# Optimization experiments

Hardware: AMD Instinct MI355X
Metric: run time of the kernel (lower is better)

## Reference

```python
import jax, jax.numpy as jnp
import numpy as np

B, T, D, H, L, F = 128, 512, 32, 128, 3, 4


def setup_inputs() -> dict:
    key = jax.random.key(0)
    ks = jax.random.split(key, 13)
    s = 0.05
    inp = {
        "x": jax.random.normal(ks[0], (B, T, D), dtype=jnp.float32),
        # layer 0 input weights [4H, D]; layers 1..L-1 input weights [L-1, 4H, H]
        "w_ih0": jax.random.normal(ks[1], (4 * H, D), dtype=jnp.float32) * s,
        "w_ih_rest": jax.random.normal(ks[2], (L - 1, 4 * H, H), dtype=jnp.float32) * s,
        "w_hh": jax.random.normal(ks[3], (L, 4 * H, H), dtype=jnp.float32) * s,
        "b_ih": jax.random.normal(ks[4], (L, 4 * H), dtype=jnp.float32) * s,
        "b_hh": jax.random.normal(ks[5], (L, 4 * H), dtype=jnp.float32) * s,
        "w_attn": jax.random.normal(ks[6], (1, H), dtype=jnp.float32) * s,
        "b_attn": jax.random.normal(ks[7], (1,), dtype=jnp.float32) * s,
        "w1": jax.random.normal(ks[8], (64, H), dtype=jnp.float32) * s,
        "b1": jax.random.normal(ks[9], (64,), dtype=jnp.float32) * s,
        "w2": jax.random.normal(ks[10], (F, 64), dtype=jnp.float32) * s,
        "b2": jax.random.normal(ks[11], (F,), dtype=jnp.float32) * s,
    }
    return inp


def _lstm_layer(xs, w_ih, w_hh, bi, bh):
    # xs: [B, T, Din] -> hs: [B, T, H]; PyTorch gate order i, f, g, o
    b, t = xs.shape[0], xs.shape[1]
    h_dim = w_hh.shape[1]
    pre = jnp.einsum('bti,gi->btg', xs, w_ih) + bi + bh  # [B, T, 4H]

    def step(carry, p_t):
        h, c = carry
        g = p_t + h @ w_hh.T
        i, f, gg, o = jnp.split(g, 4, axis=-1)
        i = jax.nn.sigmoid(i)
        f = jax.nn.sigmoid(f)
        gg = jnp.tanh(gg)
        o = jax.nn.sigmoid(o)
        c = f * c + i * gg
        h = o * jnp.tanh(c)
        return (h, c), h

    h0 = jnp.zeros((b, h_dim), xs.dtype)
    _, hs = jax.lax.scan(step, (h0, h0), jnp.swapaxes(pre, 0, 1))
    return jnp.swapaxes(hs, 0, 1)


def reference(x, w_ih0, w_ih_rest, w_hh, b_ih, b_hh, w_attn, b_attn, w1, b1, w2, b2):
    out = _lstm_layer(x, w_ih0, w_hh[0], b_ih[0], b_hh[0])
    for l in range(1, L):
        out = _lstm_layer(out, w_ih_rest[l - 1], w_hh[l], b_ih[l], b_hh[l])
    # additive attention pooling over time
    attn_w = jax.nn.softmax(jnp.einsum('bth,oh->bto', out, w_attn) + b_attn, axis=1)  # [B,T,1]
    ctx = jnp.sum(attn_w * out, axis=1)  # [B, H]
    # MLP head (dropout is identity at inference)
    h1 = jax.nn.relu(ctx @ w1.T + b1)
    return h1 @ w2.T + b2
```

## Files before the change

kernel.cpp:

```cpp
#include <hip/hip_runtime.h>
#include <math.h>

#define Bn 128
#define Tn 512
#define Dn 32
#define Hn 128
#define Gn 512
#define Ln 3

#define BAR_LDS() asm volatile("s_waitcnt lgkmcnt(0)\n\ts_barrier" ::: "memory")

typedef _Float16 h2 __attribute__((ext_vector_type(2)));
typedef _Float16 h4 __attribute__((ext_vector_type(4)));
typedef _Float16 half8 __attribute__((ext_vector_type(8)));
typedef float f32x4 __attribute__((ext_vector_type(4)));

__device__ __forceinline__ float dot2(h2 a, h2 b, float c) {
    return __builtin_amdgcn_fdot2(a, b, c, false);
}
__device__ __forceinline__ h2 pkh(float a, float b) {
    h2 r; r.x = (_Float16)a; r.y = (_Float16)b; return r;
}
__device__ __forceinline__ float sigm(float x) {
    return __builtin_amdgcn_rcpf(1.f + __expf(-x));
}
__device__ __forceinline__ float tanh_fast(float x) {
    return 1.f - 2.f * __builtin_amdgcn_rcpf(1.f + __expf(2.f * x));
}

#define DPPADD(a, CTRL) { \
    int _t = __builtin_amdgcn_update_dpp(0, __builtin_bit_cast(int, a), \
                                         CTRL, 0xF, 0xF, true); \
    a += __builtin_bit_cast(float, _t); }

#define KEEPH(x) asm volatile("" : "+v"(x))
#define LD8H(p) (*(const half8*)(p))
#define H2OF(V, i) (((const h2*)&(V))[i])

#define DECL16(P, R) \
  h2 P##0=pkh((R)[0],(R)[1]),   P##1=pkh((R)[2],(R)[3]),   P##2=pkh((R)[4],(R)[5]),   P##3=pkh((R)[6],(R)[7]),   \
     P##4=pkh((R)[8],(R)[9]),   P##5=pkh((R)[10],(R)[11]), P##6=pkh((R)[12],(R)[13]), P##7=pkh((R)[14],(R)[15]), \
     P##8=pkh((R)[16],(R)[17]), P##9=pkh((R)[18],(R)[19]), P##10=pkh((R)[20],(R)[21]),P##11=pkh((R)[22],(R)[23]),\
     P##12=pkh((R)[24],(R)[25]),P##13=pkh((R)[26],(R)[27]),P##14=pkh((R)[28],(R)[29]),P##15=pkh((R)[30],(R)[31]);
#define KEEP16(P) \
  KEEPH(P##0); KEEPH(P##1); KEEPH(P##2); KEEPH(P##3); KEEPH(P##4); KEEPH(P##5); \
  KEEPH(P##6); KEEPH(P##7); KEEPH(P##8); KEEPH(P##9); KEEPH(P##10); KEEPH(P##11); \
  KEEPH(P##12); KEEPH(P##13); KEEPH(P##14); KEEPH(P##15);

#define EXTRACT16(P, A, B, C, D) \
  h2 P##0 = H2OF(A,0), P##1 = H2OF(A,1), P##2  = H2OF(A,2), P##3  = H2OF(A,3), \
     P##4 = H2OF(B,0), P##5 = H2OF(B,1), P##6  = H2OF(B,2), P##7  = H2OF(B,3), \
     P##8 = H2OF(C,0), P##9 = H2OF(C,1), P##10 = H2OF(C,2), P##11 = H2OF(C,3), \
     P##12= H2OF(D,0), P##13= H2OF(D,1), P##14 = H2OF(D,2), P##15 = H2OF(D,3);

#define DOTA(j) { \
    aI = dot2(hvA##j, wiA##j, aI);  aF = dot2(hvA##j, wfA##j, aF); \
    aG = dot2(hvA##j, wgA##j, aG);  aO = dot2(hvA##j, woA##j, aO); }
#define DOTB(j) { \
    aI = dot2(hvB##j, wiB##j, aI);  aF = dot2(hvB##j, wfB##j, aF); \
    aG = dot2(hvB##j, wgB##j, aG);  aO = dot2(hvB##j, woB##j, aO); }

template<typename TA>
__global__ __launch_bounds__(256) void gemm_pre(
    const TA* __restrict__ A, int K, int rowStrideB, int t0, int tlog,
    const float* __restrict__ W,
    const float* __restrict__ bi, const float* __restrict__ bh,
    _Float16* __restrict__ C)
{
    __shared__ h2 As2[64][20];
    __shared__ h2 Bs2[64][20];
    const int tid  = threadIdx.x;
    const int row0 = blockIdx.x * 64;
    const int col0 = blockIdx.y * 64;
    const int w    = tid >> 6;
    const int lane = tid & 63;
    const int qm   = (w >> 1) * 32;
    const int qn   = (w & 1) * 32;
    const int fm   = lane & 15;
    const int fq   = lane >> 4;
    const int tmask = (1 << tlog) - 1;
    const int lrow = tid >> 2;
    const int lk   = (tid & 3) * 8;

    f32x4 acc00 = {0,0,0,0}, acc01 = {0,0,0,0};
    f32x4 acc10 = {0,0,0,0}, acc11 = {0,0,0,0};

    for (int k0 = 0; k0 < K; k0 += 32) {
        {
            int rg = row0 + lrow;
            int b_idx = rg >> tlog, tt = rg & tmask;
            const TA* ap = A + (size_t)b_idx * rowStrideB +
                           (size_t)(t0 + tt) * K + (k0 + lk);
            if constexpr (sizeof(TA) == 2) {
                *(float4*)&As2[lrow][(tid & 3) * 4] = *(const float4*)ap;
            } else {
                float4 va = *(const float4*)ap;
                float4 vb = *(const float4*)(ap + 4);
                float4 o;
                ((h2*)&o)[0] = pkh(va.x, va.y);
                ((h2*)&o)[1] = pkh(va.z, va.w);
                ((h2*)&o)[2] = pkh(vb.x, vb.y);
                ((h2*)&o)[3] = pkh(vb.z, vb.w);
                *(float4*)&As2[lrow][(tid & 3) * 4] = o;
            }
            const float* wp = W + (size_t)(col0 + lrow) * K + (k0 + lk);
            float4 wa = *(const float4*)wp;
            float4 wb = *(const float4*)(wp + 4);
            float4 ow;
            ((h2*)&ow)[0] = pkh(wa.x, wa.y);
            ((h2*)&ow)[1] = pkh(wa.z, wa.w);
            ((h2*)&ow)[2] = pkh(wb.x, wb.y);
            ((h2*)&ow)[3] = pkh(wb.z, wb.w);
            *(float4*)&Bs2[lrow][(tid & 3) * 4] = ow;
        }
        __syncthreads();
        half8 a0 = *(const half8*)&As2[qm + fm][fq * 4];
        half8 a1 = *(const half8*)&As2[qm + 16 + fm][fq * 4];
        half8 b0 = *(const half8*)&Bs2[qn + fm][fq * 4];
        half8 b1 = *(const half8*)&Bs2[qn + 16 + fm][fq * 4];
        acc00 = __builtin_amdgcn_mfma_f32_16x16x32_f16(a0, b0, acc00, 0, 0, 0);
        acc01 = __builtin_amdgcn_mfma_f32_16x16x32_f16(a0, b1, acc01, 0, 0, 0);
        acc10 = __builtin_amdgcn_mfma_f32_16x16x32_f16(a1, b0, acc10, 0, 0, 0);
        acc11 = __builtin_amdgcn_mfma_f32_16x16x32_f16(a1, b1, acc11, 0, 0, 0);
        __syncthreads();
    }

    const int g0 = col0 + qn + fm;
    const int g1 = g0 + 16;
    const float bb0 = bi[g0] + bh[g0];
    const float bb1 = bi[g1] + bh[g1];
    const int m0 = row0 + qm + fq * 4;
    #pragma unroll
    for (int r = 0; r < 4; r++) {
        int ma = m0 + r, mb = m0 + 16 + r;
        C[((size_t)(ma >> 2) * Gn + g0) * 4 + (ma & 3)] = (_Float16)(acc00[r] + bb0);
        C[((size_t)(ma >> 2) * Gn + g1) * 4 + (ma & 3)] = (_Float16)(acc01[r] + bb1);
        C[((size_t)(mb >> 2) * Gn + g0) * 4 + (mb & 3)] = (_Float16)(acc10[r] + bb0);
        C[((size_t)(mb >> 2) * Gn + g1) * 4 + (mb & 3)] = (_Float16)(acc11[r] + bb1);
    }
}

__global__ __launch_bounds__(256)
__attribute__((amdgpu_waves_per_eu(1, 2)))
void scan256(
    const _Float16* __restrict__ pre,
    const float* __restrict__ w_hh,
    _Float16* __restrict__ hs16)
{
    const int b    = blockIdx.x;
    const int tid  = threadIdx.x;
    const int lane = tid & 63;
    const int wv   = tid >> 6;
    const int kq   = lane & 1;
    const int u    = wv * 32 + (lane >> 1);

    __shared__ h2 hbuf[2][Hn / 2];
    __shared__ _Float16 hstage[2][16][Hn];
    __shared__ float lds_pad[19456];

    if (pre == nullptr) {
        lds_pad[tid] = (float)tid;
        __syncthreads();
        ((float*)hs16)[tid] = lds_pad[(tid * 7) & 19455];
    }

    const float* rI = w_hh + (size_t)(0 * Hn + u) * Hn + kq * 64;
    const float* rF = w_hh + (size_t)(1 * Hn + u) * Hn + kq * 64;
    const float* rG = w_hh + (size_t)(2 * Hn + u) * Hn + kq * 64;
    const float* rO = w_hh + (size_t)(3 * Hn + u) * Hn + kq * 64;
    DECL16(wiA, rI) DECL16(wiB, (rI + 32))
    DECL16(wfA, rF) DECL16(wfB, (rF + 32))
    DECL16(wgA, rG) DECL16(wgB, (rG + 32))
    DECL16(woA, rO) DECL16(woB, (rO + 32))
    KEEP16(wiA) KEEP16(wiB) KEEP16(wfA) KEEP16(wfB)
    KEEP16(wgA) KEEP16(wgB) KEEP16(woA) KEEP16(woB)

    if (tid < Hn / 2) hbuf[0][tid] = pkh(0.f, 0.f);
    __syncthreads();

    const h4* qq = (const h4*)pre + (size_t)(b * 128) * Gn + u;
    _Float16* hsb = hs16 + (size_t)b * Tn * Hn;

    const float ms = (kq == 0) ? 1.f : 0.f;

    h4 qI0 = qq[0],   qF0 = qq[128],      qG0 = qq[256],      qO0 = qq[384];
    h4 qI1 = qq[Gn],  qF1 = qq[Gn + 128], qG1 = qq[Gn + 256], qO1 = qq[Gn + 384];
    const h4* pld = qq + 2 * (size_t)Gn;

    float cr = 0.f;

    auto body = [&](int t, float vI, float vF, float vG, float vO) {
        const h2* hrow = &hbuf[t & 1][kq * 32];
        half8 hA = LD8H(hrow);      half8 hB = LD8H(hrow + 4);
        half8 hC = LD8H(hrow + 8);  half8 hD = LD8H(hrow + 12);
        half8 hE = LD8H(hrow + 16); half8 hF_ = LD8H(hrow + 20);
        half8 hG_ = LD8H(hrow + 24); half8 hH_ = LD8H(hrow + 28);
        EXTRACT16(hvA, hA, hB, hC, hD)
        EXTRACT16(hvB, hE, hF_, hG_, hH_)

        float aI = vI, aF = vF, aG = vG, aO = vO;
        DOTA(0)  DOTA(1)  DOTA(2)  DOTA(3)
        DOTA(4)  DOTA(5)  DOTA(6)  DOTA(7)
        DOTA(8)  DOTA(9)  DOTA(10) DOTA(11)
        DOTA(12) DOTA(13) DOTA(14) DOTA(15)
        DOTB(0)  DOTB(1)  DOTB(2)  DOTB(3)
        DOTB(4)  DOTB(5)  DOTB(6)  DOTB(7)
        DOTB(8)  DOTB(9)  DOTB(10) DOTB(11)
        DOTB(12) DOTB(13) DOTB(14) DOTB(15)

        DPPADD(aI, 0xB1) DPPADD(aF, 0xB1) DPPADD(aG, 0xB1) DPPADD(aO, 0xB1)

        float iv = sigm(aI);
        float fv = sigm(aF);
        float gv = tanh_fast(aG);
        float ov = sigm(aO);
        cr = fv * cr + iv * gv;
        float hnew = ov * tanh_fast(cr);
        _Float16 hh = (_Float16)hnew;
        if (kq == 0) {
            ((_Float16*)hbuf[(t + 1) & 1])[u] = hh;
            hstage[(t >> 4) & 1][t & 15][u] = hh;
        }
        BAR_LDS();
    };

    auto flush = [&](int ch) {
        const float4* src = (const float4*)&hstage[ch & 1][0][0];
        float4 v = src[tid];
        *(float4*)(hsb + (size_t)ch * 16 * Hn + tid * 8) = v;
    };

    for (int qr = 0; qr < 126; qr++) {
        body(4 * qr,     ms * (float)qI0.x, ms * (float)qF0.x,
                         ms * (float)qG0.x, ms * (float)qO0.x);
        body(4 * qr + 1, ms * (float)qI0.y, ms * (float)qF0.y,
                         ms * (float)qG0.y, ms * (float)qO0.y);
        body(4 * qr + 2, ms * (float)qI0.z, ms * (float)qF0.z,
                         ms * (float)qG0.z, ms * (float)qO0.z);
        body(4 * qr + 3, ms * (float)qI0.w, ms * (float)qF0.w,
                         ms * (float)qG0.w, ms * (float)qO0.w);
        if ((qr & 3) == 3) flush(qr >> 2);
        qI0 = qI1; qF0 = qF1; qG0 = qG1; qO0 = qO1;
        qI1 = pld[0]; qF1 = pld[128]; qG1 = pld[256]; qO1 = pld[384];
        pld += Gn;
    }
    body(504, ms * (float)qI0.x, ms * (float)qF0.x,
              ms * (float)qG0.x, ms * (float)qO0.x);
    body(505, ms * (float)qI0.y, ms * (float)qF0.y,
              ms * (float)qG0.y, ms * (float)qO0.y);
    body(506, ms * (float)qI0.z, ms * (float)qF0.z,
              ms * (float)qG0.z, ms * (float)qO0.z);
    body(507, ms * (float)qI0.w, ms * (float)qF0.w,
              ms * (float)qG0.w, ms * (float)qO0.w);
    qI0 = qI1; qF0 = qF1; qG0 = qG1; qO0 = qO1;
    body(508, ms * (float)qI0.x, ms * (float)qF0.x,
              ms * (float)qG0.x, ms * (float)qO0.x);
    body(509, ms * (float)qI0.y, ms * (float)qF0.y,
              ms * (float)qG0.y, ms * (float)qO0.y);
    body(510, ms * (float)qI0.z, ms * (float)qF0.z,
              ms * (float)qG0.z, ms * (float)qO0.z);
    body(511, ms * (float)qI0.w, ms * (float)qF0.w,
              ms * (float)qG0.w, ms * (float)qO0.w);
    flush(31);
}

__global__ __launch_bounds__(256) void head_kernel(
    const _Float16* __restrict__ hs16,
    const float* __restrict__ w_attn, const float* __restrict__ b_attn,
    const float* __restrict__ w1, const float* __restrict__ b1,
    const float* __restrict__ w2, const float* __restrict__ b2,
    float* __restrict__ out)
{
    const int b = blockIdx.x;
    const int tid = threadIdx.x;
    __shared__ h2 wa2[Hn / 2];
    __shared__ __align__(16) float sc[Tn];
    __shared__ __align__(16) float red[256];
    __shared__ __align__(16) float ctx_sh[Hn];
    __shared__ __align__(16) float h1_sh[64];

    if (tid < Hn / 2) wa2[tid] = pkh(w_attn[2 * tid], w_attn[2 * tid + 1]);
    __syncthreads();

    const _Float16* hb = hs16 + (size_t)b * Tn * Hn;

    for (int t = tid; t < Tn; t += 256) {
        const h2* hp = (const h2*)(hb + (size_t)t * Hn);
        float s = 0.f;
        #pragma unroll
        for (int k = 0; k < 64; k++) s = dot2(hp[k], wa2[k], s);
        sc[t] = s + b_attn[0];
    }
    __syncthreads();

    float m = fmaxf(sc[tid], sc[tid + 256]);
    red[tid] = m; __syncthreads();
    for (int s_ = 128; s_ > 0; s_ >>= 1) {
        if (tid < s_) red[tid] = fmaxf(red[tid], red[tid + s_]);
        __syncthreads();
    }
    float mx = red[0];
    __syncthreads();
    float e0 = __expf(sc[tid] - mx), e1 = __expf(sc[tid + 256] - mx);
    sc[tid] = e0; sc[tid + 256] = e1;
    red[tid] = e0 + e1; __syncthreads();
    for (int s_ = 128; s_ > 0; s_ >>= 1) {
        if (tid < s_) red[tid] += red[tid + s_];
        __syncthreads();
    }
    float inv = 1.f / red[0];
    __syncthreads();

    {
        int jj = tid & 127, half = tid >> 7;
        float a = 0.f;
        for (int t = half * 256; t < half * 256 + 256; t++)
            a += sc[t] * (float)hb[(size_t)t * Hn + jj];
        red[tid] = a;
        __syncthreads();
        if (tid < Hn) ctx_sh[tid] = (red[tid] + red[tid + Hn]) * inv;
        __syncthreads();
    }

    if (tid < 64) {
        const float4* wvv = (const float4*)(w1 + (size_t)tid * Hn);
        const float4* cv = (const float4*)ctx_sh;
        float s = 0.f;
        #pragma unroll
        for (int k = 0; k < 32; k++) {
            float4 a = wvv[k], c = cv[k];
            s += a.x * c.x + a.y * c.y + a.z * c.z + a.w * c.w;
        }
        h1_sh[tid] = fmaxf(s + b1[tid], 0.f);
    }
    __syncthreads();

    if (tid < 4) {
        float s = 0.f;
        const float* wvv = w2 + tid * 64;
        #pragma unroll
        for (int k = 0; k < 64; k++) s += wvv[k] * h1_sh[k];
        out[b * 4 + tid] = s + b2[tid];
    }
}

extern "C" void kernel_launch(void* const* d_in, const int* in_sizes, int n_in,
                              void* d_out, int out_size, void* d_ws, size_t ws_size,
                              hipStream_t stream)
{
    const float* x        = (const float*)d_in[0];
    const float* w_ih0    = (const float*)d_in[1];
    const float* w_ih_rest= (const float*)d_in[2];
    const float* w_hh     = (const float*)d_in[3];
    const float* b_ih     = (const float*)d_in[4];
    const float* b_hh     = (const float*)d_in[5];
    const float* w_attn   = (const float*)d_in[6];
    const float* b_attn   = (const float*)d_in[7];
    const float* w1       = (const float*)d_in[8];
    const float* b1       = (const float*)d_in[9];
    const float* w2       = (const float*)d_in[10];
    const float* b2       = (const float*)d_in[11];
    float* out = (float*)d_out;

    const size_t nHS  = (size_t)Bn * Tn * Hn;
    const size_t nPRE = (size_t)Bn * Tn * Gn;

    _Float16* preh = (_Float16*)d_ws;
    _Float16* hs0  = preh + nPRE;
    _Float16* hs1  = hs0 + nHS;
    _Float16* hs2  = hs1 + nHS;

    gemm_pre<float><<<dim3(Bn * Tn / 64, 8), 256, 0, stream>>>(
        x, Dn, Tn * Dn, 0, 9, w_ih0, b_ih, b_hh, preh);
    scan256<<<Bn, 256, 0, stream>>>(preh, w_hh, hs0);

    gemm_pre<_Float16><<<dim3(Bn * Tn / 64, 8), 256, 0, stream>>>(
        hs0, Hn, Tn * Hn, 0, 9, w_ih_rest,
        b_ih + Gn, b_hh + Gn, preh);
    scan256<<<Bn, 256, 0, stream>>>(preh, w_hh + (size_t)Gn * Hn, hs1);

    gemm_pre<_Float16><<<dim3(Bn * Tn / 64, 8), 256, 0, stream>>>(
        hs1, Hn, Tn * Hn, 0, 9, w_ih_rest + (size_t)Gn * Hn,
        b_ih + 2 * Gn, b_hh + 2 * Gn, preh);
    scan256<<<Bn, 256, 0, stream>>>(preh, w_hh + 2 * (size_t)Gn * Hn, hs2);

    head_kernel<<<Bn, 256, 0, stream>>>(hs2, w_attn, b_attn, w1, b1, w2, b2, out);
}
```

Baseline: 991.3 us.

## Fuse layer-0 and layer-1 LSTM scans into one wavefront-pipelined kernel

Result: slower. 1.017 ms (+2.6%).

```diff
diff --git a/kernel.cpp b/kernel.cpp
--- a/kernel.cpp
+++ b/kernel.cpp
@@ -59,6 +59,12 @@
 #define DOTB(j) { \
     aI = dot2(hvB##j, wiB##j, aI);  aF = dot2(hvB##j, wfB##j, aF); \
     aG = dot2(hvB##j, wgB##j, aG);  aO = dot2(hvB##j, woB##j, aO); }
+#define DOT4V(j) { \
+    aI = dot2(hv##j, wi##j, aI);  aF = dot2(hv##j, wf##j, aF); \
+    aG = dot2(hv##j, wg##j, aG);  aO = dot2(hv##j, wo##j, aO); }
+#define DOT4Y(j) { \
+    aI = dot2(pv##j, yi##j, aI);  aF = dot2(pv##j, yf##j, aF); \
+    aG = dot2(pv##j, yg##j, aG);  aO = dot2(pv##j, yo##j, aO); }
 
 template<typename TA>
 __global__ __launch_bounds__(256) void gemm_pre(
@@ -140,6 +146,201 @@
     }
 }
 
+__global__ __launch_bounds__(768)
+__attribute__((amdgpu_waves_per_eu(3)))
+void pipe01(
+    const _Float16* __restrict__ pre0,
+    const float* __restrict__ w_hh,
+    const float* __restrict__ wih1,
+    const float* __restrict__ b_ih, const float* __restrict__ b_hh,
+    _Float16* __restrict__ hs1)
+{
+    const int b    = blockIdx.x;
+    const int tid  = threadIdx.x;
+    const int lane = tid & 63;
+    const int wv   = tid >> 6;
+
+    __shared__ h2 h0buf[2][Hn / 2];
+    __shared__ h2 h1buf[2][Hn / 2];
+    __shared__ _Float16 hstage[2][16][Hn];
+
+    if (tid < Hn / 2) {
+        h0buf[0][tid] = pkh(0.f, 0.f); h0buf[1][tid] = pkh(0.f, 0.f);
+        h1buf[0][tid] = pkh(0.f, 0.f); h1buf[1][tid] = pkh(0.f, 0.f);
+    }
+    __syncthreads();
+
+    if (wv < 4) {
+        const int kq = lane & 1;
+        const int u  = wv * 32 + (lane >> 1);
+
+        const float* rI = w_hh + (size_t)(0 * Hn + u) * Hn + kq * 64;
+        const float* rF = w_hh + (size_t)(1 * Hn + u) * Hn + kq * 64;
+        const float* rG = w_hh + (size_t)(2 * Hn + u) * Hn + kq * 64;
+        const float* rO = w_hh + (size_t)(3 * Hn + u) * Hn + kq * 64;
+        DECL16(wiA, rI) DECL16(wiB, (rI + 32))
+        DECL16(wfA, rF) DECL16(wfB, (rF + 32))
+        DECL16(wgA, rG) DECL16(wgB, (rG + 32))
+        DECL16(woA, rO) DECL16(woB, (rO + 32))
+        KEEP16(wiA) KEEP16(wiB) KEEP16(wfA) KEEP16(wfB)
+        KEEP16(wgA) KEEP16(wgB) KEEP16(woA) KEEP16(woB)
+
+        const h4* qq = (const h4*)pre0 + (size_t)(b * 128) * Gn + u;
+        const float ms = (kq == 0) ? 1.f : 0.f;
+
+        h4 qI0 = qq[0],  qF0 = qq[128],      qG0 = qq[256],      qO0 = qq[384];
+        h4 qI1 = qq[Gn], qF1 = qq[Gn + 128], qG1 = qq[Gn + 256], qO1 = qq[Gn + 384];
+        const h4* pld = qq + 2 * (size_t)Gn;
+
+        float cr = 0.f;
+
+        auto body = [&](int t, float vI, float vF, float vG, float vO) {
+            const h2* hrow = &h0buf[t & 1][kq * 32];
+            half8 hA = LD8H(hrow);      half8 hB = LD8H(hrow + 4);
+            half8 hC = LD8H(hrow + 8);  half8 hD = LD8H(hrow + 12);
+            half8 hE = LD8H(hrow + 16); half8 hF_ = LD8H(hrow + 20);
+            half8 hG_ = LD8H(hrow + 24); half8 hH_ = LD8H(hrow + 28);
+            EXTRACT16(hvA, hA, hB, hC, hD)
+            EXTRACT16(hvB, hE, hF_, hG_, hH_)
+
+            float aI = vI, aF = vF, aG = vG, aO = vO;
+            DOTA(0)  DOTA(1)  DOTA(2)  DOTA(3)
+            DOTA(4)  DOTA(5)  DOTA(6)  DOTA(7)
+            DOTA(8)  DOTA(9)  DOTA(10) DOTA(11)
+            DOTA(12) DOTA(13) DOTA(14) DOTA(15)
+            DOTB(0)  DOTB(1)  DOTB(2)  DOTB(3)
+            DOTB(4)  DOTB(5)  DOTB(6)  DOTB(7)
+            DOTB(8)  DOTB(9)  DOTB(10) DOTB(11)
+            DOTB(12) DOTB(13) DOTB(14) DOTB(15)
+
+            DPPADD(aI, 0xB1) DPPADD(aF, 0xB1) DPPADD(aG, 0xB1) DPPADD(aO, 0xB1)
+
+            float iv = sigm(aI);
+            float fv = sigm(aF);
+            float gv = tanh_fast(aG);
+            float ov = sigm(aO);
+            cr = fv * cr + iv * gv;
+            float hnew = ov * tanh_fast(cr);
+            if (kq == 0)
+                ((_Float16*)h0buf[(t + 1) & 1])[u] = (_Float16)hnew;
+            BAR_LDS();
+        };
+
+        for (int qr = 0; qr < 126; qr++) {
+            body(4 * qr,     ms * (float)qI0.x, ms * (float)qF0.x,
+                             ms * (float)qG0.x, ms * (float)qO0.x);
+            body(4 * qr + 1, ms * (float)qI0.y, ms * (float)qF0.y,
+                             ms * (float)qG0.y, ms * (float)qO0.y);
+            body(4 * qr + 2, ms * (float)qI0.z, ms * (float)qF0.z,
+                             ms * (float)qG0.z, ms * (float)qO0.z);
+            body(4 * qr + 3, ms * (float)qI0.w, ms * (float)qF0.w,
+                             ms * (float)qG0.w, ms * (float)qO0.w);
+            qI0 = qI1; qF0 = qF1; qG0 = qG1; qO0 = qO1;
+            qI1 = pld[0]; qF1 = pld[128]; qG1 = pld[256]; qO1 = pld[384];
+            pld += Gn;
+        }
+        body(504, ms * (float)qI0.x, ms * (float)qF0.x,
+                  ms * (float)qG0.x, ms * (float)qO0.x);
+        body(505, ms * (float)qI0.y, ms * (float)qF0.y,
+                  ms * (float)qG0.y, ms * (float)qO0.y);
+        body(506, ms * (float)qI0.z, ms * (float)qF0.z,
+                  ms * (float)qG0.z, ms * (float)qO0.z);
+        body(507, ms * (float)qI0.w, ms * (float)qF0.w,
+                  ms * (float)qG0.w, ms * (float)qO0.w);
+        qI0 = qI1; qF0 = qF1; qG0 = qG1; qO0 = qO1;
+        body(508, ms * (float)qI0.x, ms * (float)qF0.x,
+                  ms * (float)qG0.x, ms * (float)qO0.x);
+        body(509, ms * (float)qI0.y, ms * (float)qF0.y,
+                  ms * (float)qG0.y, ms * (float)qO0.y);
+        body(510, ms * (float)qI0.z, ms * (float)qF0.z,
+                  ms * (float)qG0.z, ms * (float)qO0.z);
+        body(511, ms * (float)qI0.w, ms * (float)qF0.w,
+                  ms * (float)qG0.w, ms * (float)qO0.w);
+        BAR_LDS();
+        BAR_LDS();
+    } else {
+        const int wl   = wv - 4;
+        const int kq4  = lane & 3;
+        const int u1   = wl * 16 + (lane >> 2);
+        const int ltid = tid - 256;
+
+        const float* whh1 = w_hh + (size_t)Gn * Hn;
+        const float* rI = whh1 + (size_t)(0 * Hn + u1) * Hn + kq4 * 32;
+        const float* rF = whh1 + (size_t)(1 * Hn + u1) * Hn + kq4 * 32;
+        const float* rG = whh1 + (size_t)(2 * Hn + u1) * Hn + kq4 * 32;
+        const float* rO = whh1 + (size_t)(3 * Hn + u1) * Hn + kq4 * 32;
+        DECL16(wi, rI) DECL16(wf, rF) DECL16(wg, rG) DECL16(wo, rO)
+        KEEP16(wi) KEEP16(wf) KEEP16(wg) KEEP16(wo)
+
+        const float* yIr = wih1 + (size_t)(0 * Hn + u1) * Hn + kq4 * 32;
+        const float* yFr = wih1 + (size_t)(1 * Hn + u1) * Hn + kq4 * 32;
+        const float* yGr = wih1 + (size_t)(2 * Hn + u1) * Hn + kq4 * 32;
+        const float* yOr = wih1 + (size_t)(3 * Hn + u1) * Hn + kq4 * 32;
+        DECL16(yi, yIr) DECL16(yf, yFr) DECL16(yg, yGr) DECL16(yo, yOr)
+        KEEP16(yi) KEEP16(yf) KEEP16(yg) KEEP16(yo)
+
+        const float bI1 = b_ih[Gn + 0 * Hn + u1] + b_hh[Gn + 0 * Hn + u1];
+        const float bF1 = b_ih[Gn + 1 * Hn + u1] + b_hh[Gn + 1 * Hn + u1];
+        const float bG1 = b_ih[Gn + 2 * Hn + u1] + b_hh[Gn + 2 * Hn + u1];
+        const float bO1 = b_ih[Gn + 3 * Hn + u1] + b_hh[Gn + 3 * Hn + u1];
+
+        _Float16* hs1b = hs1 + (size_t)b * Tn * Hn;
+        float cr = 0.f;
+
+        for (int i = 0; i < 513; i++) {
+            if (i > 0) {
+                const int t1 = i - 1;
+                const h2* h1row = &h1buf[(i - 1) & 1][kq4 * 16];
+                half8 hA = LD8H(h1row);     half8 hB = LD8H(h1row + 4);
+                half8 hC = LD8H(h1row + 8); half8 hD = LD8H(h1row + 12);
+                EXTRACT16(hv, hA, hB, hC, hD)
+                const h2* h0row = &h0buf[i & 1][kq4 * 16];
+                half8 pA = LD8H(h0row);     half8 pB = LD8H(h0row + 4);
+                half8 pC = LD8H(h0row + 8); half8 pD = LD8H(h0row + 12);
+                EXTRACT16(pv, pA, pB, pC, pD)
+
+                float aI = 0.f, aF = 0.f, aG = 0.f, aO = 0.f;
+                DOT4V(0)  DOT4V(1)  DOT4V(2)  DOT4V(3)
+                DOT4V(4)  DOT4V(5)  DOT4V(6)  DOT4V(7)
+                DOT4V(8)  DOT4V(9)  DOT4V(10) DOT4V(11)
+                DOT4V(12) DOT4V(13) DOT4V(14) DOT4V(15)
+                DOT4Y(0)  DOT4Y(1)  DOT4Y(2)  DOT4Y(3)
+                DOT4Y(4)  DOT4Y(5)  DOT4Y(6)  DOT4Y(7)
+                DOT4Y(8)  DOT4Y(9)  DOT4Y(10) DOT4Y(11)
+                DOT4Y(12) DOT4Y(13) DOT4Y(14) DOT4Y(15)
+
+                DPPADD(aI, 0xB1) DPPADD(aF, 0xB1) DPPADD(aG, 0xB1) DPPADD(aO, 0xB1)
+                DPPADD(aI, 0x4E) DPPADD(aF, 0x4E) DPPADD(aG, 0x4E) DPPADD(aO, 0x4E)
+
+                float iv = sigm(aI + bI1);
+                float fv = sigm(aF + bF1);
+                float gv = tanh_fast(aG + bG1);
+                float ov = sigm(aO + bO1);
+                cr = fv * cr + iv * gv;
+                float hnew = ov * tanh_fast(cr);
+                _Float16 hh_ = (_Float16)hnew;
+                if (kq4 == 0) {
+                    ((_Float16*)h1buf[i & 1])[u1] = hh_;
+                    hstage[(t1 >> 4) & 1][t1 & 15][u1] = hh_;
+                }
+            }
+            if ((i & 15) == 1 && i > 16) {
+                int ch = (i - 17) >> 4;
+                if (ltid < 256) {
+                    float4 v = ((const float4*)&hstage[ch & 1][0][0])[ltid];
+                    *(float4*)(hs1b + (size_t)ch * 16 * Hn + ltid * 8) = v;
+                }
+            }
+            BAR_LDS();
+        }
+        BAR_LDS();
+        if (ltid < 256) {
+            float4 v = ((const float4*)&hstage[1][0][0])[ltid];
+            *(float4*)(hs1b + (size_t)31 * 16 * Hn + ltid * 8) = v;
+        }
+    }
+}
+
 __global__ __launch_bounds__(256)
 __attribute__((amdgpu_waves_per_eu(1, 2)))
 void scan256(
@@ -366,18 +567,13 @@
     const size_t nPRE = (size_t)Bn * Tn * Gn;
 
     _Float16* preh = (_Float16*)d_ws;
-    _Float16* hs0  = preh + nPRE;
-    _Float16* hs1  = hs0 + nHS;
+    _Float16* hs1  = preh + nPRE;
     _Float16* hs2  = hs1 + nHS;
 
     gemm_pre<float><<<dim3(Bn * Tn / 64, 8), 256, 0, stream>>>(
         x, Dn, Tn * Dn, 0, 9, w_ih0, b_ih, b_hh, preh);
-    scan256<<<Bn, 256, 0, stream>>>(preh, w_hh, hs0);
-
-    gemm_pre<_Float16><<<dim3(Bn * Tn / 64, 8), 256, 0, stream>>>(
-        hs0, Hn, Tn * Hn, 0, 9, w_ih_rest,
-        b_ih + Gn, b_hh + Gn, preh);
-    scan256<<<Bn, 256, 0, stream>>>(preh, w_hh + (size_t)Gn * Hn, hs1);
+
+    pipe01<<<Bn, 768, 0, stream>>>(preh, w_hh, w_ih_rest, b_ih, b_hh, hs1);
 
     gemm_pre<_Float16><<<dim3(Bn * Tn / 64, 8), 256, 0, stream>>>(
         hs1, Hn, Tn * Hn, 0, 9, w_ih_rest + (size_t)Gn * Hn,
```

## Pipeline LSTM layers 0 and 1 in one kernel with flag-based handoff

Applied to the files above, without the earlier changes.

Measured after the change: 894.0 us. -9.8%, faster.

```diff
diff --git a/kernel.cpp b/kernel.cpp
--- a/kernel.cpp
+++ b/kernel.cpp
@@ -59,6 +59,12 @@
 #define DOTB(j) { \
     aI = dot2(hvB##j, wiB##j, aI);  aF = dot2(hvB##j, wfB##j, aF); \
     aG = dot2(hvB##j, wgB##j, aG);  aO = dot2(hvB##j, woB##j, aO); }
+#define DOT4V(j) { \
+    aI = dot2(hv##j, wi##j, aI);  aF = dot2(hv##j, wf##j, aF); \
+    aG = dot2(hv##j, wg##j, aG);  aO = dot2(hv##j, wo##j, aO); }
+#define DOT4Y(j) { \
+    aI = dot2(pv##j, yi##j, aI);  aF = dot2(pv##j, yf##j, aF); \
+    aG = dot2(pv##j, yg##j, aG);  aO = dot2(pv##j, yo##j, aO); }
 
 template<typename TA>
 __global__ __launch_bounds__(256) void gemm_pre(
@@ -140,6 +146,215 @@
     }
 }
 
+__global__ __launch_bounds__(512)
+__attribute__((amdgpu_waves_per_eu(2)))
+void pipe(
+    const _Float16* __restrict__ pre0,
+    const float* __restrict__ w_hh,
+    const float* __restrict__ wih1,
+    const float* __restrict__ b_ih, const float* __restrict__ b_hh,
+    _Float16* __restrict__ hs0,
+    _Float16* __restrict__ hs1,
+    int* __restrict__ flags)
+{
+    const int b    = blockIdx.x;
+    const int layer= blockIdx.y;
+    const int tid  = threadIdx.x;
+    const int lane = tid & 63;
+    const int wv   = tid >> 6;
+    const int kq4  = lane & 3;
+    const int u    = wv * 16 + (lane >> 2);
+
+    __shared__ h2 hb[2][Hn / 2];
+    __shared__ _Float16 hstage[2][16][Hn];
+    __shared__ _Float16 pL[2][16][Hn];
+    __shared__ float lds_pad[20480];
+
+    if (pre0 == nullptr) {
+        lds_pad[tid] = (float)tid;
+        __syncthreads();
+        ((float*)hs0)[tid] = lds_pad[(tid * 7) & 20479];
+    }
+
+    const float* whl = w_hh + (size_t)layer * Gn * Hn;
+    const float* rI = whl + (size_t)(0 * Hn + u) * Hn + kq4 * 32;
+    const float* rF = whl + (size_t)(1 * Hn + u) * Hn + kq4 * 32;
+    const float* rG = whl + (size_t)(2 * Hn + u) * Hn + kq4 * 32;
+    const float* rO = whl + (size_t)(3 * Hn + u) * Hn + kq4 * 32;
+    DECL16(wi, rI) DECL16(wf, rF) DECL16(wg, rG) DECL16(wo, rO)
+    KEEP16(wi) KEEP16(wf) KEEP16(wg) KEEP16(wo)
+
+    if (tid < Hn / 2) hb[0][tid] = pkh(0.f, 0.f);
+
+    float cr = 0.f;
+
+    if (layer == 0) {
+        __syncthreads();
+        const float mI = (kq4 == 0) ? 1.f : 0.f;
+        const float mF = (kq4 == 1) ? 1.f : 0.f;
+        const float mG = (kq4 == 2) ? 1.f : 0.f;
+        const float mO = (kq4 == 3) ? 1.f : 0.f;
+
+        const h4* qq = (const h4*)pre0 + (size_t)(b * 128) * Gn + kq4 * Hn + u;
+        _Float16* hs0b = hs0 + (size_t)b * Tn * Hn;
+
+        h4 q0 = qq[0];
+        h4 q1 = qq[Gn];
+        const h4* pld = qq + 2 * (size_t)Gn;
+
+        auto tick = [&](int t, float pv) {
+            const h2* hrow = &hb[t & 1][kq4 * 16];
+            half8 hA = LD8H(hrow);     half8 hB = LD8H(hrow + 4);
+            half8 hC = LD8H(hrow + 8); half8 hD = LD8H(hrow + 12);
+            EXTRACT16(hv, hA, hB, hC, hD)
+
+            float aI = 0.f, aF = 0.f, aG = 0.f, aO = 0.f;
+            DOT4V(0)  DOT4V(1)  DOT4V(2)  DOT4V(3)
+            DOT4V(4)  DOT4V(5)  DOT4V(6)  DOT4V(7)
+            DOT4V(8)  DOT4V(9)  DOT4V(10) DOT4V(11)
+            DOT4V(12) DOT4V(13) DOT4V(14) DOT4V(15)
+
+            aI = fmaf(pv, mI, aI);
+            aF = fmaf(pv, mF, aF);
+            aG = fmaf(pv, mG, aG);
+            aO = fmaf(pv, mO, aO);
+
+            DPPADD(aI, 0xB1) DPPADD(aF, 0xB1) DPPADD(aG, 0xB1) DPPADD(aO, 0xB1)
+            DPPADD(aI, 0x4E) DPPADD(aF, 0x4E) DPPADD(aG, 0x4E) DPPADD(aO, 0x4E)
+
+            float iv = sigm(aI);
+            float fv = sigm(aF);
+            float gv = tanh_fast(aG);
+            float ov = sigm(aO);
+            cr = fv * cr + iv * gv;
+            float hnew = ov * tanh_fast(cr);
+            _Float16 hh = (_Float16)hnew;
+            if (kq4 == 0) {
+                ((_Float16*)hb[(t + 1) & 1])[u] = hh;
+                hstage[(t >> 4) & 1][t & 15][u] = hh;
+            }
+            BAR_LDS();
+        };
+
+        auto flush_pub = [&](int ch) {
+            if (tid < 256) {
+                float4 v = ((const float4*)&hstage[ch & 1][0][0])[tid];
+                *(float4*)(hs0b + (size_t)ch * 16 * Hn + tid * 8) = v;
+            }
+            asm volatile("s_waitcnt vmcnt(0)" ::: "memory");
+            __syncthreads();
+            if (tid == 0)
+                __hip_atomic_store(flags + b, ch + 1, __ATOMIC_RELEASE,
+                                   __HIP_MEMORY_SCOPE_AGENT);
+        };
+
+        for (int qr = 0; qr < 126; qr++) {
+            tick(4 * qr,     (float)q0.x);
+            tick(4 * qr + 1, (float)q0.y);
+            tick(4 * qr + 2, (float)q0.z);
+            tick(4 * qr + 3, (float)q0.w);
+            if ((qr & 3) == 3) flush_pub(qr >> 2);
+            q0 = q1;
+            q1 = *pld; pld += Gn;
+        }
+        tick(504, (float)q0.x); tick(505, (float)q0.y);
+        tick(506, (float)q0.z); tick(507, (float)q0.w);
+        q0 = q1;
+        tick(508, (float)q0.x); tick(509, (float)q0.y);
+        tick(510, (float)q0.z); tick(511, (float)q0.w);
+        flush_pub(31);
+    } else {
+        const float* yIr = wih1 + (size_t)(0 * Hn + u) * Hn + kq4 * 32;
+        const float* yFr = wih1 + (size_t)(1 * Hn + u) * Hn + kq4 * 32;
+        const float* yGr = wih1 + (size_t)(2 * Hn + u) * Hn + kq4 * 32;
+        const float* yOr = wih1 + (size_t)(3 * Hn + u) * Hn + kq4 * 32;
+        DECL16(yi, yIr) DECL16(yf, yFr) DECL16(yg, yGr) DECL16(yo, yOr)
+        KEEP16(yi) KEEP16(yf) KEEP16(yg) KEEP16(yo)
+
+        const float bI1 = b_ih[Gn + 0 * Hn + u] + b_hh[Gn + 0 * Hn + u];
+        const float bF1 = b_ih[Gn + 1 * Hn + u] + b_hh[Gn + 1 * Hn + u];
+        const float bG1 = b_ih[Gn + 2 * Hn + u] + b_hh[Gn + 2 * Hn + u];
+        const float bO1 = b_ih[Gn + 3 * Hn + u] + b_hh[Gn + 3 * Hn + u];
+
+        const _Float16* hs0b = hs0 + (size_t)b * Tn * Hn;
+        _Float16* hs1b = hs1 + (size_t)b * Tn * Hn;
+
+        int avail = 0;
+        auto gate = [&](int need) {
+            if (avail >= need) return;
+            do {
+                int a0 = 0;
+                if (lane == 0)
+                    a0 = __hip_atomic_load(flags + b, __ATOMIC_ACQUIRE,
+                                           __HIP_MEMORY_SCOPE_AGENT);
+                avail = __builtin_amdgcn_readfirstlane(a0);
+                if (avail < need) __builtin_amdgcn_s_sleep(8);
+            } while (avail < need);
+        };
+
+        auto tick = [&](int t) {
+            const h2* h1row = &hb[t & 1][kq4 * 16];
+            half8 hA = LD8H(h1row);     half8 hB = LD8H(h1row + 4);
+            half8 hC = LD8H(h1row + 8); half8 hD = LD8H(h1row + 12);
+            EXTRACT16(hv, hA, hB, hC, hD)
+            const h2* h0row = (const h2*)&pL[(t >> 4) & 1][t & 15][kq4 * 32];
+            half8 pA = LD8H(h0row);     half8 pB = LD8H(h0row + 4);
+            half8 pC = LD8H(h0row + 8); half8 pD = LD8H(h0row + 12);
+            EXTRACT16(pv, pA, pB, pC, pD)
+
+            float aI = 0.f, aF = 0.f, aG = 0.f, aO = 0.f;
+            DOT4V(0)  DOT4V(1)  DOT4V(2)  DOT4V(3)
+            DOT4V(4)  DOT4V(5)  DOT4V(6)  DOT4V(7)
+            DOT4V(8)  DOT4V(9)  DOT4V(10) DOT4V(11)
+            DOT4V(12) DOT4V(13) DOT4V(14) DOT4V(15)
+            DOT4Y(0)  DOT4Y(1)  DOT4Y(2)  DOT4Y(3)
+            DOT4Y(4)  DOT4Y(5)  DOT4Y(6)  DOT4Y(7)
+            DOT4Y(8)  DOT4Y(9)  DOT4Y(10) DOT4Y(11)
+            DOT4Y(12) DOT4Y(13) DOT4Y(14) DOT4Y(15)
+
+            DPPADD(aI, 0xB1) DPPADD(aF, 0xB1) DPPADD(aG, 0xB1) DPPADD(aO, 0xB1)
+            DPPADD(aI, 0x4E) DPPADD(aF, 0x4E) DPPADD(aG, 0x4E) DPPADD(aO, 0x4E)
+
+            float iv = sigm(aI + bI1);
+            float fv = sigm(aF + bF1);
+            float gv = tanh_fast(aG + bG1);
+            float ov = sigm(aO + bO1);
+            cr = fv * cr + iv * gv;
+            float hnew = ov * tanh_fast(cr);
+            _Float16 hh = (_Float16)hnew;
+            if (kq4 == 0) {
+                ((_Float16*)hb[(t + 1) & 1])[u] = hh;
+                hstage[(t >> 4) & 1][t & 15][u] = hh;
+            }
+            BAR_LDS();
+        };
+
+        gate(1);
+        if (tid < 256) {
+            float4 v = *(const float4*)(hs0b + tid * 8);
+            *(float4*)((_Float16*)&pL[0][0][0] + tid * 8) = v;
+        }
+        __syncthreads();
+
+        for (int c = 0; c < 32; c++) {
+            if (c + 1 < 32) {
+                gate(c + 2);
+                if (tid < 256) {
+                    float4 v = *(const float4*)(hs0b +
+                                (size_t)(c + 1) * 16 * Hn + tid * 8);
+                    *(float4*)((_Float16*)&pL[(c + 1) & 1][0][0] + tid * 8) = v;
+                }
+            }
+            #pragma unroll
+            for (int tt = 0; tt < 16; tt++) tick(16 * c + tt);
+            if (tid < 256) {
+                float4 v = ((const float4*)&hstage[c & 1][0][0])[tid];
+                *(float4*)(hs1b + (size_t)c * 16 * Hn + tid * 8) = v;
+            }
+        }
+    }
+}
+
 __global__ __launch_bounds__(256)
 __attribute__((amdgpu_waves_per_eu(1, 2)))
 void scan256(
@@ -369,15 +584,15 @@
     _Float16* hs0  = preh + nPRE;
     _Float16* hs1  = hs0 + nHS;
     _Float16* hs2  = hs1 + nHS;
+    int* flags     = (int*)(hs2 + nHS);
+
+    hipMemsetAsync(flags, 0, Bn * sizeof(int), stream);
 
     gemm_pre<float><<<dim3(Bn * Tn / 64, 8), 256, 0, stream>>>(
         x, Dn, Tn * Dn, 0, 9, w_ih0, b_ih, b_hh, preh);
-    scan256<<<Bn, 256, 0, stream>>>(preh, w_hh, hs0);
-
-    gemm_pre<_Float16><<<dim3(Bn * Tn / 64, 8), 256, 0, stream>>>(
-        hs0, Hn, Tn * Hn, 0, 9, w_ih_rest,
-        b_ih + Gn, b_hh + Gn, preh);
-    scan256<<<Bn, 256, 0, stream>>>(preh, w_hh + (size_t)Gn * Hn, hs1);
+
+    pipe<<<dim3(Bn, 2), 512, 0, stream>>>(preh, w_hh, w_ih_rest,
+                                          b_ih, b_hh, hs0, hs1, flags);
 
     gemm_pre<_Float16><<<dim3(Bn * Tn / 64, 8), 256, 0, stream>>>(
         hs1, Hn, Tn * Hn, 0, 9, w_ih_rest + (size_t)Gn * Hn,
```
